# Performance work log

Hardware: AMD Instinct MI355X
Metric: run time of the kernel (lower is better)

The kernel has to match this reference:

```python
import jax, jax.numpy as jnp
import numpy as np

EPS = 1e-12
ALPHA = 100.0

def _l2norm(v, axis):
    n = jnp.sqrt(jnp.sum(v * v, axis=axis, keepdims=True))
    return v / jnp.maximum(n, EPS)

def setup_inputs() -> dict:
    key = jax.random.key(0)
    k1, k2, k3 = jax.random.split(key, 3)
    N, C, H, W, K = 64, 128, 64, 64, 64
    x = jax.random.normal(k1, (N, C, H, W), dtype=jnp.float32)
    xyz = jax.random.normal(k2, (N, 3, H * W), dtype=jnp.float32)
    centroids = jax.random.uniform(k3, (K, C), dtype=jnp.float32)
    # conv params are initialized from centroids as in _init_params
    conv_w = 2.0 * ALPHA * centroids              # [K, C] (1x1 kernel squeezed)
    conv_b = -ALPHA * jnp.linalg.norm(centroids, axis=1)  # [K]
    return {"x": x, "xyz": xyz, "centroids": centroids, "conv_w": conv_w, "conv_b": conv_b}

def reference(x, xyz, centroids, conv_w, conv_b):
    N, C = x.shape[:2]
    K = centroids.shape[0]
    # descriptor-wise L2 normalization over channel dim
    x = _l2norm(x, axis=1)
    xf = x.reshape(N, C, -1)                      # [N, C, P]
    # 1x1 conv == channel matmul; softmax over clusters
    logits = jnp.einsum('kc,ncp->nkp', conv_w, xf) + conv_b[None, :, None]
    a = jax.nn.softmax(logits, axis=1)            # [N, K, P]
    # vlad[n,k,c] = sum_p a*x  -  (sum_p a) * centroid  (algebraically equal to
    # the original broadcasted-residual construction, without the NKCP tensor)
    vlad = jnp.einsum('nkp,ncp->nkc', a, xf) - a.sum(axis=-1)[..., None] * centroids[None]
    vlad = _l2norm(vlad, axis=2)                  # intra-normalization
    vlad = vlad.reshape(N, -1)
    vlad = _l2norm(vlad, axis=1)
    return vlad[..., None]                        # [N, K*C, 1]
```

## Files before the change

### kernel.cpp

```cpp
#include <hip/hip_runtime.h>
#include <math.h>

#define N_ 64
#define C_ 128
#define K_ 64
#define P_ 4096
#define PT 32
#define TILES_PER_N 8
#define PB (P_ / TILES_PER_N)
#define NSUB (PB / PT)

typedef __attribute__((ext_vector_type(8))) short short8;
typedef __attribute__((ext_vector_type(4))) float f32x4;

union U4S8 { uint4 u4; unsigned int u[4]; short8 s; };

__device__ __forceinline__ unsigned int pair_hi(float a, float b) {
    return (__float_as_uint(b) & 0xffff0000u) | (__float_as_uint(a) >> 16);
}
__device__ __forceinline__ float lo_part(float f) {
    return f - __uint_as_float(__float_as_uint(f) & 0xffff0000u);
}

#define MFMA16(a, b, c) __builtin_amdgcn_mfma_f32_16x16x32_bf16(a, b, c, 0, 0, 0)

__device__ __forceinline__ int pmask(int p) { return (p & 7) ^ ((p >> 3) & 3); }

__global__ __launch_bounds__(256, 2)
void netvlad_main(const float* __restrict__ x,
                  const float* __restrict__ conv_w,
                  const float* __restrict__ conv_b,
                  float* __restrict__ acc_part,
                  float* __restrict__ asum_part,
                  int use_atomic)
{
    __shared__ unsigned int xhi [PT * 64];
    __shared__ unsigned int xlo [PT * 64];
    __shared__ unsigned int xthi[C_ * 20];
    __shared__ unsigned int xtlo[C_ * 20];
    __shared__ unsigned int ahi_[K_ * 20];
    __shared__ unsigned int alo_[K_ * 20];
    __shared__ float        asl [PT * 68];
    __shared__ float        red2[4 * 33];
    __shared__ float        rn_ [PT];

    const int t  = threadIdx.x;
    const int wv = t >> 6;
    const int l  = t & 63;
    const int n    = blockIdx.x >> 3;
    const int tile = blockIdx.x & 7;

    const int mrow = l & 15;
    const int kq   = l >> 4;

    const int ppq = t & 7;
    const int cq  = t >> 3;

    const int kseg = l >> 3;
    const int scol = 8 * wv + (l & 7);

    const int ntp = wv & 1;
    const int mt0 = 2 * (wv >> 1);

    short8 whi[2][4], wlo[2][4];
    #pragma unroll
    for (int mtl = 0; mtl < 2; ++mtl) {
        const float* wr = conv_w + (size_t)((mt0 + mtl) * 16 + mrow) * C_;
        #pragma unroll
        for (int s = 0; s < 4; ++s) {
            U4S8 h, lo;
            #pragma unroll
            for (int j = 0; j < 4; ++j) {
                float f0 = wr[s * 32 + kq * 8 + 2 * j];
                float f1 = wr[s * 32 + kq * 8 + 2 * j + 1];
                h.u[j]  = pair_hi(f0, f1);
                lo.u[j] = pair_hi(lo_part(f0), lo_part(f1));
            }
            whi[mtl][s] = h.s; wlo[mtl][s] = lo.s;
        }
    }
    float cb8[8];
    #pragma unroll
    for (int i = 0; i < 8; ++i) cb8[i] = conv_b[kseg * 8 + i];

    f32x4 accC[4][2];
    #pragma unroll
    for (int mt = 0; mt < 4; ++mt)
        #pragma unroll
        for (int ntl = 0; ntl < 2; ++ntl) accC[mt][ntl] = (f32x4){0.f, 0.f, 0.f, 0.f};
    float asum_acc[8];
    #pragma unroll
    for (int i = 0; i < 8; ++i) asum_acc[i] = 0.f;

    const float* xb = x + ((size_t)n * C_) * P_ + tile * PB + 4 * ppq;

    float4 ld[4];
    #pragma unroll
    for (int cc = 0; cc < 4; ++cc)
        ld[cc] = *(const float4*)(xb + (size_t)(4 * cq + cc) * P_);

    for (int sub = 0; sub < NSUB; ++sub) {
        __syncthreads();

        {
            const float* lf = (const float*)ld;
            #pragma unroll
            for (int cc = 0; cc < 4; ++cc) {
                float4 v = ld[cc];
                int c = 4 * cq + cc;
                uint2 wh; wh.x = pair_hi(v.x, v.y); wh.y = pair_hi(v.z, v.w);
                *(uint2*)(xthi + c * 20 + 2 * ppq) = wh;
                uint2 wl; wl.x = pair_hi(lo_part(v.x), lo_part(v.y));
                wl.y = pair_hi(lo_part(v.z), lo_part(v.w));
                *(uint2*)(xtlo + c * 20 + 2 * ppq) = wl;
            }
            float ssq[4];
            #pragma unroll
            for (int j = 0; j < 4; ++j) {
                int p = 4 * ppq + j;
                int ch = cq >> 1;
                int chp = (ch & 8) | ((ch ^ pmask(p)) & 7);
                int base = p * 64 + (chp << 2) + ((cq & 1) << 1);
                float f0 = lf[0 * 4 + j], f1 = lf[1 * 4 + j];
                float f2 = lf[2 * 4 + j], f3 = lf[3 * 4 + j];
                uint2 wh; wh.x = pair_hi(f0, f1); wh.y = pair_hi(f2, f3);
                *(uint2*)(xhi + base) = wh;
                uint2 wl; wl.x = pair_hi(lo_part(f0), lo_part(f1));
                wl.y = pair_hi(lo_part(f2), lo_part(f3));
                *(uint2*)(xlo + base) = wl;
                ssq[j] = f0 * f0 + f1 * f1 + f2 * f2 + f3 * f3;
            }
            #pragma unroll
            for (int j = 0; j < 4; ++j) {
                ssq[j] += __shfl_xor(ssq[j], 8);
                ssq[j] += __shfl_xor(ssq[j], 16);
                ssq[j] += __shfl_xor(ssq[j], 32);
            }
            if (l < 8) {
                #pragma unroll
                for (int j = 0; j < 4; ++j) red2[wv * 33 + 4 * l + j] = ssq[j];
            }
        }
        if (sub + 1 < NSUB) {
            #pragma unroll
            for (int cc = 0; cc < 4; ++cc)
                ld[cc] = *(const float4*)(xb + (size_t)(4 * cq + cc) * P_ + (sub + 1) * PT);
        }
        __syncthreads();

        if (t < PT) {
            float ss = red2[t] + red2[33 + t] + red2[66 + t] + red2[99 + t];
            rn_[t] = 1.f / fmaxf(sqrtf(ss), 1e-12f);
        }

        {
            const int prow = ntp * 16 + mrow;
            const int msk = pmask(prow);
            f32x4 a0 = (f32x4){0.f, 0.f, 0.f, 0.f};
            f32x4 a1 = (f32x4){0.f, 0.f, 0.f, 0.f};
            #pragma unroll
            for (int s = 0; s < 4; ++s) {
                int ch = s * 4 + kq;
                int chp = (ch & 8) | ((ch ^ msk) & 7);
                int idx = prow * 64 + (chp << 2);
                U4S8 bh, bl;
                bh.u4 = *(const uint4*)(xhi + idx);
                bl.u4 = *(const uint4*)(xlo + idx);
                a0 = MFMA16(whi[0][s], bh.s, a0);
                a0 = MFMA16(whi[0][s], bl.s, a0);
                a0 = MFMA16(wlo[0][s], bh.s, a0);
                a1 = MFMA16(whi[1][s], bh.s, a1);
                a1 = MFMA16(whi[1][s], bl.s, a1);
                a1 = MFMA16(wlo[1][s], bh.s, a1);
            }
            *(f32x4*)(asl + prow * 68 + (mt0    ) * 16 + kq * 4) = a0;
            *(f32x4*)(asl + prow * 68 + (mt0 + 1) * 16 + kq * 4) = a1;
        }
        __syncthreads();

        {
            float rnv = rn_[scol];
            f32x4 q0 = *(const f32x4*)(asl + scol * 68 + kseg * 8);
            f32x4 q1 = *(const f32x4*)(asl + scol * 68 + kseg * 8 + 4);
            float lv[8];
            #pragma unroll
            for (int i = 0; i < 4; ++i) { lv[i] = q0[i] * rnv + cb8[i]; }
            #pragma unroll
            for (int i = 0; i < 4; ++i) { lv[4 + i] = q1[i] * rnv + cb8[4 + i]; }
            float m = lv[0];
            #pragma unroll
            for (int i = 1; i < 8; ++i) m = fmaxf(m, lv[i]);
            float s = 0.f;
            #pragma unroll
            for (int i = 0; i < 8; ++i) s += __expf(lv[i] - m);
            #pragma unroll
            for (int off = 8; off <= 32; off <<= 1) {
                float mo = __shfl_xor(m, off);
                float so = __shfl_xor(s, off);
                float Mn = fmaxf(m, mo);
                s = s * __expf(m - Mn) + so * __expf(mo - Mn);
                m = Mn;
            }
            float inv = 1.f / s;
            const int p2 = scol >> 1;
            #pragma unroll
            for (int i = 0; i < 8; ++i) {
                float a = __expf(lv[i] - m) * inv;
                asum_acc[i] += a;
                float av = a * rnv;
                float pav = __shfl_xor(av, 1);
                if ((l & 1) == 0) {
                    int k = kseg * 8 + i;
                    int chp = wv ^ (kseg & 3);
                    int off = k * 20 + (chp << 2) + (p2 & 3);
                    ahi_[off] = pair_hi(av, pav);
                    alo_[off] = pair_hi(lo_part(av), lo_part(pav));
                }
            }
        }
        __syncthreads();

        {
            U4S8 ah[4], al[4];
            #pragma unroll
            for (int mt = 0; mt < 4; ++mt) {
                int ar = mt * 16 + mrow;
                int chp = kq ^ ((ar >> 3) & 3);
                int idx = ar * 20 + (chp << 2);
                ah[mt].u4 = *(const uint4*)(ahi_ + idx);
                al[mt].u4 = *(const uint4*)(alo_ + idx);
            }
            #pragma unroll
            for (int ntl = 0; ntl < 2; ++ntl) {
                int cr = (2 * wv + ntl) * 16 + mrow;
                int xi = cr * 20 + kq * 4;
                U4S8 xh, xl2;
                xh.u4  = *(const uint4*)(xthi + xi);
                xl2.u4 = *(const uint4*)(xtlo + xi);
                #pragma unroll
                for (int mt = 0; mt < 4; ++mt) {
                    accC[mt][ntl] = MFMA16(ah[mt].s, xh.s,  accC[mt][ntl]);
                    accC[mt][ntl] = MFMA16(ah[mt].s, xl2.s, accC[mt][ntl]);
                    accC[mt][ntl] = MFMA16(al[mt].s, xh.s,  accC[mt][ntl]);
                }
            }
        }
    }

    __syncthreads();
    #pragma unroll
    for (int i = 0; i < 8; ++i) {
        asum_acc[i] += __shfl_xor(asum_acc[i], 1);
        asum_acc[i] += __shfl_xor(asum_acc[i], 2);
        asum_acc[i] += __shfl_xor(asum_acc[i], 4);
    }
    float* fred = (float*)xhi;
    if ((l & 7) == 0) {
        #pragma unroll
        for (int i = 0; i < 8; ++i) fred[wv * 64 + kseg * 8 + i] = asum_acc[i];
    }
    if (!use_atomic) {
        float* dst = acc_part + (size_t)blockIdx.x * K_ * C_;
        #pragma unroll
        for (int mt = 0; mt < 4; ++mt)
            #pragma unroll
            for (int r = 0; r < 4; ++r)
                #pragma unroll
                for (int ntl = 0; ntl < 2; ++ntl)
                    dst[(mt * 16 + kq * 4 + r) * C_ + (2 * wv + ntl) * 16 + mrow] =
                        accC[mt][ntl][r];
    } else {
        float* dst = acc_part + (size_t)n * K_ * C_;
        #pragma unroll
        for (int mt = 0; mt < 4; ++mt)
            #pragma unroll
            for (int r = 0; r < 4; ++r)
                #pragma unroll
                for (int ntl = 0; ntl < 2; ++ntl)
                    atomicAdd(dst + (mt * 16 + kq * 4 + r) * C_ + (2 * wv + ntl) * 16 + mrow,
                              accC[mt][ntl][r]);
    }
    __syncthreads();
    if (t < K_) {
        float v = fred[t] + fred[64 + t] + fred[128 + t] + fred[192 + t];
        if (use_atomic) atomicAdd(asum_part + n * K_ + t, v);
        else            asum_part[(size_t)blockIdx.x * K_ + t] = v;
    }
}

__global__ __launch_bounds__(256, 4)
void netvlad_finalize(const float* __restrict__ acc_part,
                      const float* __restrict__ asum_part,
                      const float* __restrict__ centroids,
                      float* __restrict__ out,
                      int npart)
{
    __shared__ float wred[4];
    const int t = threadIdx.x;
    const int n = blockIdx.x;
    const int k = t >> 2;
    const int part = t & 3;

    float a_k = 0.f;
    for (int s = 0; s < npart; ++s)
        a_k += asum_part[(size_t)(n * npart + s) * K_ + k];

    float4 vals[8];
    #pragma unroll
    for (int i = 0; i < 8; ++i) vals[i] = make_float4(0.f, 0.f, 0.f, 0.f);
    for (int s = 0; s < npart; ++s) {
        const float4* av = (const float4*)(acc_part
            + ((size_t)(n * npart + s) * K_ + k) * C_ + part * 32);
        #pragma unroll
        for (int i = 0; i < 8; ++i) {
            float4 a = av[i];
            vals[i].x += a.x; vals[i].y += a.y;
            vals[i].z += a.z; vals[i].w += a.w;
        }
    }

    const float4* cenv = (const float4*)(centroids + k * C_ + part * 32);
    float loc = 0.f;
    #pragma unroll
    for (int i = 0; i < 8; ++i) {
        float4 cv = cenv[i];
        float4 v = vals[i];
        v.x -= a_k * cv.x; v.y -= a_k * cv.y;
        v.z -= a_k * cv.z; v.w -= a_k * cv.w;
        vals[i] = v;
        loc += v.x * v.x + v.y * v.y + v.z * v.z + v.w * v.w;
    }
    loc += __shfl_xor(loc, 1);
    loc += __shfl_xor(loc, 2);
    float rk = 1.f / fmaxf(sqrtf(loc), 1e-12f);

    float tot = 0.f;
    #pragma unroll
    for (int i = 0; i < 8; ++i) {
        float4 v = vals[i];
        v.x *= rk; v.y *= rk; v.z *= rk; v.w *= rk;
        vals[i] = v;
        tot += v.x * v.x + v.y * v.y + v.z * v.z + v.w * v.w;
    }
    #pragma unroll
    for (int o = 1; o < 64; o <<= 1) tot += __shfl_xor(tot, o);
    if ((t & 63) == 0) wred[t >> 6] = tot;
    __syncthreads();
    float T = wred[0] + wred[1] + wred[2] + wred[3];
    float rtot = 1.f / fmaxf(sqrtf(T), 1e-12f);

    float4* outv = (float4*)(out + ((size_t)n * K_ + k) * C_ + part * 32);
    #pragma unroll
    for (int i = 0; i < 8; ++i) {
        float4 v = vals[i];
        v.x *= rtot; v.y *= rtot; v.z *= rtot; v.w *= rtot;
        outv[i] = v;
    }
}

extern "C" void kernel_launch(void* const* d_in, const int* in_sizes, int n_in,
                              void* d_out, int out_size, void* d_ws, size_t ws_size,
                              hipStream_t stream)
{
    const float* x      = (const float*)d_in[0];
    const float* cent   = (const float*)d_in[2];
    const float* conv_w = (const float*)d_in[3];
    const float* conv_b = (const float*)d_in[4];
    float* out = (float*)d_out;

    const int nblk = N_ * TILES_PER_N;
    size_t need = (size_t)nblk * K_ * C_ * sizeof(float)
                + (size_t)nblk * K_ * sizeof(float);
    int use_atomic = (ws_size >= need) ? 0 : 1;
    int npart = use_atomic ? 1 : TILES_PER_N;

    float* acc_part  = (float*)d_ws;
    float* asum_part = acc_part + (size_t)(use_atomic ? N_ : nblk) * K_ * C_;

    if (use_atomic) {
        size_t zbytes = ((size_t)N_ * K_ * C_ + (size_t)N_ * K_) * sizeof(float);
        hipMemsetAsync(d_ws, 0, zbytes, stream);
    }

    hipLaunchKernelGGL(netvlad_main, dim3(nblk), dim3(256), 0, stream,
                       x, conv_w, conv_b, acc_part, asum_part, use_atomic);
    hipLaunchKernelGGL(netvlad_finalize, dim3(N_), dim3(256), 0, stream,
                       acc_part, asum_part, cent, out, npart);
}
```

Before: 222.1 us.

## Compute softmax directly from MFMA accumulators and double tiles per sample

The conv-logit MFMA results are no longer staged through a shared-memory logits buffer. Each wave now runs the softmax partial max and sum on its accumulator registers and exchanges only per-column (max, sum) stats across the two wave halves through a small shared array. The per-column norm is read directly from a transposed red2 layout, which removes one serial step. Tiles per sample rise from 8 to 16 and occupancy is raised to 3 blocks, which gives more blocks but also more partials for the finalize kernel to reduce.

```diff
diff --git a/kernel.cpp b/kernel.cpp
--- a/kernel.cpp
+++ b/kernel.cpp
@@ -6,7 +6,7 @@
 #define K_ 64
 #define P_ 4096
 #define PT 32
-#define TILES_PER_N 8
+#define TILES_PER_N 16
 #define PB (P_ / TILES_PER_N)
 #define NSUB (PB / PT)
 
@@ -26,7 +26,7 @@
 
 __device__ __forceinline__ int pmask(int p) { return (p & 7) ^ ((p >> 3) & 3); }
 
-__global__ __launch_bounds__(256, 2)
+__global__ __launch_bounds__(256, 3)
 void netvlad_main(const float* __restrict__ x,
                   const float* __restrict__ conv_w,
                   const float* __restrict__ conv_b,
@@ -40,15 +40,15 @@
     __shared__ unsigned int xtlo[C_ * 20];
     __shared__ unsigned int ahi_[K_ * 20];
     __shared__ unsigned int alo_[K_ * 20];
-    __shared__ float        asl [PT * 68];
-    __shared__ float        red2[4 * 33];
-    __shared__ float        rn_ [PT];
+    __shared__ float        red2[PT * 4];
+    __shared__ float2       stats[PT * 2];
+    __shared__ float        fredw[2 * K_];
 
     const int t  = threadIdx.x;
     const int wv = t >> 6;
     const int l  = t & 63;
-    const int n    = blockIdx.x >> 3;
-    const int tile = blockIdx.x & 7;
+    const int n    = blockIdx.x >> 4;
+    const int tile = blockIdx.x & 15;
 
     const int mrow = l & 15;
     const int kq   = l >> 4;
@@ -56,11 +56,10 @@
     const int ppq = t & 7;
     const int cq  = t >> 3;
 
-    const int kseg = l >> 3;
-    const int scol = 8 * wv + (l & 7);
-
     const int ntp = wv & 1;
-    const int mt0 = 2 * (wv >> 1);
+    const int mth = wv >> 1;
+    const int mt0 = 2 * mth;
+    const int pcol = ntp * 16 + mrow;
 
     short8 whi[2][4], wlo[2][4];
     #pragma unroll
@@ -81,7 +80,8 @@
     }
     float cb8[8];
     #pragma unroll
-    for (int i = 0; i < 8; ++i) cb8[i] = conv_b[kseg * 8 + i];
+    for (int i = 0; i < 8; ++i)
+        cb8[i] = conv_b[32 * mth + 16 * (i >> 2) + 4 * kq + (i & 3)];
 
     f32x4 accC[4][2];
     #pragma unroll
@@ -138,7 +138,8 @@
             }
             if (l < 8) {
                 #pragma unroll
-                for (int j = 0; j < 4; ++j) red2[wv * 33 + 4 * l + j] = ssq[j];
+                for (int j = 0; j < 4; ++j)
+                    red2[(4 * (l & 7) + j) * 4 + wv] = ssq[j];
             }
         }
         if (sub + 1 < NSUB) {
@@ -148,21 +149,18 @@
         }
         __syncthreads();
 
-        if (t < PT) {
-            float ss = red2[t] + red2[33 + t] + red2[66 + t] + red2[99 + t];
-            rn_[t] = 1.f / fmaxf(sqrtf(ss), 1e-12f);
-        }
-
+        float4 rr = *(const float4*)(red2 + pcol * 4);
+        float rnv = 1.f / fmaxf(sqrtf(rr.x + rr.y + rr.z + rr.w), 1e-12f);
+
+        f32x4 a0 = (f32x4){0.f, 0.f, 0.f, 0.f};
+        f32x4 a1 = (f32x4){0.f, 0.f, 0.f, 0.f};
         {
-            const int prow = ntp * 16 + mrow;
-            const int msk = pmask(prow);
-            f32x4 a0 = (f32x4){0.f, 0.f, 0.f, 0.f};
-            f32x4 a1 = (f32x4){0.f, 0.f, 0.f, 0.f};
+            const int msk = pmask(pcol);
             #pragma unroll
             for (int s = 0; s < 4; ++s) {
                 int ch = s * 4 + kq;
                 int chp = (ch & 8) | ((ch ^ msk) & 7);
-                int idx = prow * 64 + (chp << 2);
+                int idx = pcol * 64 + (chp << 2);
                 U4S8 bh, bl;
                 bh.u4 = *(const uint4*)(xhi + idx);
                 bl.u4 = *(const uint4*)(xlo + idx);
@@ -173,45 +171,45 @@
                 a1 = MFMA16(whi[1][s], bl.s, a1);
                 a1 = MFMA16(wlo[1][s], bh.s, a1);
             }
-            *(f32x4*)(asl + prow * 68 + (mt0    ) * 16 + kq * 4) = a0;
-            *(f32x4*)(asl + prow * 68 + (mt0 + 1) * 16 + kq * 4) = a1;
-        }
+        }
+
+        float lv[8];
+        #pragma unroll
+        for (int r = 0; r < 4; ++r) { lv[r] = a0[r] * rnv + cb8[r]; }
+        #pragma unroll
+        for (int r = 0; r < 4; ++r) { lv[4 + r] = a1[r] * rnv + cb8[4 + r]; }
+        float m = lv[0];
+        #pragma unroll
+        for (int i = 1; i < 8; ++i) m = fmaxf(m, lv[i]);
+        float s = 0.f;
+        #pragma unroll
+        for (int i = 0; i < 8; ++i) s += __expf(lv[i] - m);
+        #pragma unroll
+        for (int off = 16; off <= 32; off <<= 1) {
+            float mo = __shfl_xor(m, off);
+            float so = __shfl_xor(s, off);
+            float Mn = fmaxf(m, mo);
+            s = s * __expf(m - Mn) + so * __expf(mo - Mn);
+            m = Mn;
+        }
+        if (kq == 0) stats[pcol * 2 + mth] = make_float2(m, s);
         __syncthreads();
 
         {
-            float rnv = rn_[scol];
-            f32x4 q0 = *(const f32x4*)(asl + scol * 68 + kseg * 8);
-            f32x4 q1 = *(const f32x4*)(asl + scol * 68 + kseg * 8 + 4);
-            float lv[8];
-            #pragma unroll
-            for (int i = 0; i < 4; ++i) { lv[i] = q0[i] * rnv + cb8[i]; }
-            #pragma unroll
-            for (int i = 0; i < 4; ++i) { lv[4 + i] = q1[i] * rnv + cb8[4 + i]; }
-            float m = lv[0];
-            #pragma unroll
-            for (int i = 1; i < 8; ++i) m = fmaxf(m, lv[i]);
-            float s = 0.f;
-            #pragma unroll
-            for (int i = 0; i < 8; ++i) s += __expf(lv[i] - m);
-            #pragma unroll
-            for (int off = 8; off <= 32; off <<= 1) {
-                float mo = __shfl_xor(m, off);
-                float so = __shfl_xor(s, off);
-                float Mn = fmaxf(m, mo);
-                s = s * __expf(m - Mn) + so * __expf(mo - Mn);
-                m = Mn;
-            }
-            float inv = 1.f / s;
-            const int p2 = scol >> 1;
+            float4 st = *(const float4*)(stats + pcol * 2);
+            float M = fmaxf(st.x, st.z);
+            float S = st.y * __expf(st.x - M) + st.w * __expf(st.z - M);
+            float inv = 1.f / S;
+            const int p2 = 8 * ntp + (mrow >> 1);
             #pragma unroll
             for (int i = 0; i < 8; ++i) {
-                float a = __expf(lv[i] - m) * inv;
+                float a = __expf(lv[i] - M) * inv;
                 asum_acc[i] += a;
                 float av = a * rnv;
                 float pav = __shfl_xor(av, 1);
-                if ((l & 1) == 0) {
-                    int k = kseg * 8 + i;
-                    int chp = wv ^ (kseg & 3);
+                if ((mrow & 1) == 0) {
+                    int k = 32 * mth + 16 * (i >> 2) + 4 * kq + (i & 3);
+                    int chp = (p2 >> 2) ^ ((k >> 3) & 3);
                     int off = k * 20 + (chp << 2) + (p2 & 3);
                     ahi_[off] = pair_hi(av, pav);
                     alo_[off] = pair_hi(lo_part(av), lo_part(pav));
@@ -253,11 +251,14 @@
         asum_acc[i] += __shfl_xor(asum_acc[i], 1);
         asum_acc[i] += __shfl_xor(asum_acc[i], 2);
         asum_acc[i] += __shfl_xor(asum_acc[i], 4);
-    }
-    float* fred = (float*)xhi;
-    if ((l & 7) == 0) {
-        #pragma unroll
-        for (int i = 0; i < 8; ++i) fred[wv * 64 + kseg * 8 + i] = asum_acc[i];
+        asum_acc[i] += __shfl_xor(asum_acc[i], 8);
+    }
+    if (mrow == 0) {
+        #pragma unroll
+        for (int i = 0; i < 8; ++i) {
+            int k = 32 * mth + 16 * (i >> 2) + 4 * kq + (i & 3);
+            fredw[ntp * K_ + k] = asum_acc[i];
+        }
     }
     if (!use_atomic) {
         float* dst = acc_part + (size_t)blockIdx.x * K_ * C_;
@@ -282,7 +283,7 @@
     }
     __syncthreads();
     if (t < K_) {
-        float v = fred[t] + fred[64 + t] + fred[128 + t] + fred[192 + t];
+        float v = fredw[t] + fredw[K_ + t];
         if (use_atomic) atomicAdd(asum_part + n * K_ + t, v);
         else            asum_part[(size_t)blockIdx.x * K_ + t] = v;
     }
```

New measurement: 353.3 us. 59.1% more time.
